# Kernel optimization log

Hardware: AMD Instinct MI355X
Metric: run time of the kernel (lower is better)

## Reference

```python
import jax, jax.numpy as jnp
import numpy as np

B, SI, ST, D = 2, 1024, 512, 2048
H, KV, HD = 16, 4, 128
E, F, TOPK = 8, 1024, 2
EPS = 1e-6


def _rms(x, w):
    x32 = x.astype(jnp.float32)
    y = x32 * jax.lax.rsqrt(jnp.mean(x32 * x32, axis=-1, keepdims=True) + EPS)
    return y.astype(x.dtype) * w


def _rope(x, cos, sin):
    # x: [B,S,h,HD]; cos/sin: [S,HD//2]. Complex-pair rotation (use_real=False path):
    # pairs (x[2i], x[2i+1]) treated as complex, multiplied by e^{i theta}.
    xr, xi = x[..., 0::2], x[..., 1::2]
    c = cos[None, :, None, :]
    s = sin[None, :, None, :]
    out_r = xr * c - xi * s
    out_i = xr * s + xi * c
    return jnp.stack([out_r, out_i], axis=-1).reshape(x.shape)


def setup_inputs() -> dict:
    key = jax.random.key(0)
    ks = jax.random.split(key, 12)
    def w(k, shape, fan_in):
        return jax.random.normal(k, shape, jnp.float32) * (fan_in ** -0.5)
    pos_i = np.arange(SI)[:, None].astype(np.float32)
    pos_t = np.arange(ST)[:, None].astype(np.float32)
    inv = (1.0 / (10000.0 ** (np.arange(0, HD, 2).astype(np.float32) / HD)))[None, :]
    return {
        'hidden_states': jax.random.normal(ks[0], (B, SI, D), jnp.float32),
        'encoder_hidden_states': jax.random.normal(ks[1], (B, ST, D), jnp.float32),
        'img_cos': jnp.asarray(np.cos(pos_i * inv), jnp.float32),
        'img_sin': jnp.asarray(np.sin(pos_i * inv), jnp.float32),
        'txt_cos': jnp.asarray(np.cos(pos_t * inv), jnp.float32),
        'txt_sin': jnp.asarray(np.sin(pos_t * inv), jnp.float32),
        'norm1_w': jnp.ones((D,), jnp.float32),
        'norm2_w': jnp.ones((D,), jnp.float32),
        'wq': w(ks[2], (D, H * HD), D),
        'wk': w(ks[3], (D, KV * HD), D),
        'wv': w(ks[4], (D, KV * HD), D),
        'wk_txt': w(ks[5], (D, KV * HD), D),
        'wv_txt': w(ks[6], (D, KV * HD), D),
        'wo': w(ks[7], (H * HD, D), H * HD),
        'q_norm_w': jnp.ones((HD,), jnp.float32),
        'k_norm_w': jnp.ones((HD,), jnp.float32),
        'added_k_norm_w': jnp.ones((HD,), jnp.float32),
        'router_w': w(ks[8], (D, E), D),
        'gate_up_proj': w(ks[9], (E, D, 2 * F), D),
        'down_proj': w(ks[10], (E, F, D), F),
    }


def reference(hidden_states, encoder_hidden_states, img_cos, img_sin, txt_cos, txt_sin,
              norm1_w, norm2_w, wq, wk, wv, wk_txt, wv_txt, wo,
              q_norm_w, k_norm_w, added_k_norm_w, router_w, gate_up_proj, down_proj):
    h = hidden_states
    # ---- cross-attn: image queries over concat(image, text) K/V, GQA + RoPE ----
    x = _rms(h, norm1_w)
    q = _rms((x @ wq).reshape(B, SI, H, HD), q_norm_w)
    k_img = _rms((x @ wk).reshape(B, SI, KV, HD), k_norm_w)
    v_img = (x @ wv).reshape(B, SI, KV, HD)
    q = _rope(q, img_cos, img_sin)
    k_img = _rope(k_img, img_cos, img_sin)
    k_txt = _rms((encoder_hidden_states @ wk_txt).reshape(B, ST, KV, HD), added_k_norm_w)
    k_txt = _rope(k_txt, txt_cos, txt_sin)
    v_txt = (encoder_hidden_states @ wv_txt).reshape(B, ST, KV, HD)
    k = jnp.concatenate([k_img, k_txt], axis=1)  # [B, SI+ST, KV, HD]
    v = jnp.concatenate([v_img, v_txt], axis=1)
    k = jnp.repeat(k, H // KV, axis=2)  # GQA repeat_interleave over heads
    v = jnp.repeat(v, H // KV, axis=2)
    scores = jnp.einsum('bqhd,bkhd->bhqk', q, k) * (HD ** -0.5)
    attn = jax.nn.softmax(scores.astype(jnp.float32), axis=-1).astype(q.dtype)
    o = jnp.einsum('bhqk,bkhd->bqhd', attn, v).reshape(B, SI, H * HD)
    h = h + o @ wo
    # ---- MoE: top-k router + packed SwiGLU experts ----
    xt = _rms(h, norm2_w).reshape(B * SI, D)
    probs = jax.nn.softmax((xt @ router_w).astype(jnp.float32), axis=-1)
    topv, topi = jax.lax.top_k(probs, TOPK)
    topv = topv / jnp.sum(topv, axis=-1, keepdims=True)
    wgt = jnp.sum(jax.nn.one_hot(topi, E, dtype=xt.dtype) * topv.astype(xt.dtype)[..., None], axis=1)  # [T,E]
    gate_up = jnp.einsum('td,edg->teg', xt, gate_up_proj)  # [T,E,2F]
    gate, up = gate_up[..., :F], gate_up[..., F:]
    act = jax.nn.silu(gate) * up
    eo = jnp.einsum('tef,efd->ted', act, down_proj)  # [T,E,D]
    moe_out = jnp.einsum('te,ted->td', wgt, eo).reshape(B, SI, D)
    return h + moe_out
```

## Files before the change

kernel.cpp:

```cpp
#include <hip/hip_runtime.h>


typedef __attribute__((ext_vector_type(8))) __bf16 bf16x8;
typedef __attribute__((ext_vector_type(8))) unsigned short u16x8;
typedef __attribute__((ext_vector_type(4))) float f32x4;

__device__ __forceinline__ unsigned short f2bf(float x) {
  unsigned u = __builtin_bit_cast(unsigned, x);
  u += 0x7fffu + ((u >> 16) & 1u);
  return (unsigned short)(u >> 16);
}
__device__ __forceinline__ float bf2f(unsigned short b) {
  return __builtin_bit_cast(float, ((unsigned)b) << 16);
}

__device__ __forceinline__ void glds16(const unsigned short* g, unsigned short* l) {
  __builtin_amdgcn_global_load_lds(
      (const __attribute__((address_space(1))) void*)g,
      (__attribute__((address_space(3))) void*)l, 16, 0, 0);
}

__device__ __forceinline__ int xcd_swz(int orig, int nwg) {
  int q = nwg >> 3, r = nwg & 7;
  int xcd = orig & 7, idx = orig >> 3;
  int base = (xcd < r) ? xcd * (q + 1) : r * (q + 1) + (xcd - r) * q;
  return base + idx;
}

struct CvtJobs {
  const float* src[8];
  unsigned short* dst[8];
  int K[8];
  int N[8];
  int off[9];
};

__global__ __launch_bounds__(256) void convert_all(CvtJobs jb)
{
  __shared__ unsigned short T[64][66];
  const int bid = blockIdx.x;
  int j = 0;
  #pragma unroll
  for (int i = 0; i < 8; ++i) if (bid >= jb.off[i + 1]) j = i + 1;
  const int local = bid - jb.off[j];
  const int K = jb.K[j], N = jb.N[j];
  const int kb = K >> 6, nb = N >> 6;
  const int kt = local % kb;
  const int rest = local / kb;
  const int nt = rest % nb, zi = rest / nb;
  const float* Wz = jb.src[j] + (size_t)zi * K * N;
  unsigned short* WTz = jb.dst[j] + (size_t)zi * K * N;
  const int k0 = kt * 64, n0 = nt * 64;
  const int tid = threadIdx.x;
  #pragma unroll
  for (int i = tid; i < 64 * 16; i += 256) {
    int k = i >> 4, n4 = (i & 15) * 4;
    float4 v = *(const float4*)&Wz[(size_t)(k0 + k) * N + n0 + n4];
    T[n4 + 0][k] = f2bf(v.x);
    T[n4 + 1][k] = f2bf(v.y);
    T[n4 + 2][k] = f2bf(v.z);
    T[n4 + 3][k] = f2bf(v.w);
  }
  __syncthreads();
  #pragma unroll
  for (int i = tid; i < 64 * 8; i += 256) {
    int n = i >> 3, k8 = (i & 7) * 8;
    *(u16x8*)&WTz[(size_t)(n0 + n) * K + k0 + k8] = *(const u16x8*)&T[n][k8];
  }
}

__global__ __launch_bounds__(256) void gemm_bb(
    const unsigned short* __restrict__ A, const unsigned short* __restrict__ BT,
    float* __restrict__ C, const float* __restrict__ resid,
    int M, int N, int K)
{
  __shared__ unsigned short As[2][128 * 64];
  __shared__ unsigned short Bs[2][128 * 64];
  const int mb = M >> 7;
  const int w = xcd_swz(blockIdx.x, gridDim.x);
  const int bm = (w % mb) * 128, bn = (w / mb) * 128;
  const int tid = threadIdx.x, lane = tid & 63, wid = tid >> 6;
  const int wm = (wid >> 1) * 64, wn = (wid & 1) * 64;
  const int l16 = lane & 15, g4 = lane >> 4;
  const int rseg = lane >> 3;
  const int csw  = ((lane & 7) ^ rseg) * 8;
  const unsigned short* aSrc[4];
  const unsigned short* bSrc[4];
  #pragma unroll
  for (int p = 0; p < 4; ++p) {
    int row = (p * 4 + wid) * 8 + rseg;
    aSrc[p] = A  + (size_t)(bm + row) * K + csw;
    bSrc[p] = BT + (size_t)(bn + row) * K + csw;
  }
  f32x4 acc[4][4] = {};
  const int NT = K >> 6;
  #pragma unroll
  for (int p = 0; p < 4; ++p) glds16(aSrc[p], &As[0][(p * 4 + wid) * 512]);
  #pragma unroll
  for (int p = 0; p < 4; ++p) glds16(bSrc[p], &Bs[0][(p * 4 + wid) * 512]);
  for (int t = 0; t < NT; ++t) {
    const int cur = t & 1;
    if (t + 1 < NT) {
      const int k0 = (t + 1) << 6;
      #pragma unroll
      for (int p = 0; p < 4; ++p) glds16(aSrc[p] + k0, &As[cur ^ 1][(p * 4 + wid) * 512]);
      #pragma unroll
      for (int p = 0; p < 4; ++p) glds16(bSrc[p] + k0, &Bs[cur ^ 1][(p * 4 + wid) * 512]);
      asm volatile("s_waitcnt vmcnt(8)" ::: "memory");
    } else {
      asm volatile("s_waitcnt vmcnt(0)" ::: "memory");
    }
    __builtin_amdgcn_s_barrier();
    __builtin_amdgcn_sched_barrier(0);
    const unsigned short* ab = &As[cur][0];
    const unsigned short* bb = &Bs[cur][0];
    #pragma unroll
    for (int ks = 0; ks < 2; ++ks) {
      bf16x8 af[4], bf[4];
      #pragma unroll
      for (int i = 0; i < 4; ++i) {
        int ra = wm + i * 16 + l16;
        int rb = wn + i * 16 + l16;
        int ch = ((ks * 4 + g4) ^ (l16 & 7)) * 8;
        af[i] = *(const bf16x8*)&ab[ra * 64 + ch];
        bf[i] = *(const bf16x8*)&bb[rb * 64 + ch];
      }
      #pragma unroll
      for (int mi = 0; mi < 4; ++mi)
        #pragma unroll
        for (int ni = 0; ni < 4; ++ni)
          acc[mi][ni] = __builtin_amdgcn_mfma_f32_16x16x32_bf16(af[mi], bf[ni], acc[mi][ni], 0, 0, 0);
    }
    __builtin_amdgcn_sched_barrier(0);
    __builtin_amdgcn_s_barrier();
  }
  const int r4 = g4 * 4;
  #pragma unroll
  for (int mi = 0; mi < 4; ++mi)
    #pragma unroll
    for (int ni = 0; ni < 4; ++ni)
      #pragma unroll
      for (int r = 0; r < 4; ++r) {
        int row = bm + wm + mi * 16 + r4 + r;
        int col = bn + wn + ni * 16 + l16;
        float v = acc[mi][ni][r];
        if (resid) v += resid[(size_t)row * N + col];
        C[(size_t)row * N + col] = v;
      }
}

__global__ __launch_bounds__(512, 1) void gemm_moe_256sk(
    const unsigned short* __restrict__ A, const unsigned short* __restrict__ BTall,
    float* __restrict__ C0, float* __restrict__ C1,
    const int* __restrict__ counts, const int* __restrict__ offsets,
    const int* __restrict__ pair_token, const unsigned short* __restrict__ zbuf,
    int gather, int K, int N)
{
  const int w = xcd_swz(blockIdx.x, gridDim.x);
  const int e = w >> 7;
  const int local = w & 127;
  const int bm = ((local >> 4) & 7) * 256;
  const int kh = (local >> 3) & 1;
  const int bn = (local & 7) * 256;
  const int cnt = counts[e];
  if (bm >= cnt) return;
  const int base = offsets[e];
  const int Kh = K >> 1;
  float* __restrict__ C = kh ? C1 : C0;
  __shared__ unsigned short As[256 * 64];
  __shared__ unsigned short Bs[256 * 64];
  __shared__ int rowmap[256];
  const int tid = threadIdx.x, lane = tid & 63, wid = tid >> 6;
  const int wr = wid >> 2, wc = wid & 3;
  const int l16 = lane & 15, g4 = lane >> 4;
  const int rseg = lane >> 3;
  const int csw  = ((lane & 7) ^ rseg) * 8;
  if (tid < 256) {
    int lr = bm + tid;
    rowmap[tid] = (lr < cnt) ? (gather ? pair_token[base + lr] : base + lr) : -1;
  }
  __syncthreads();
  const unsigned short* BT = BTall + (size_t)e * N * K;
  const unsigned short* aSrc[4];
  const unsigned short* bSrc[4];
  int aOk[4];
  #pragma unroll
  for (int p = 0; p < 4; ++p) {
    int row = (p * 8 + wid) * 8 + rseg;
    int tok = rowmap[row];
    aOk[p] = (tok >= 0);
    aSrc[p] = aOk[p] ? (A + (size_t)tok * K + kh * Kh + csw) : (zbuf + csw);
    bSrc[p] = BT + (size_t)(bn + row) * K + kh * Kh + csw;
  }
  f32x4 acc[8][4] = {};
  const int NT = Kh >> 6;
  for (int t = 0; t < NT; ++t) {
    const int k0 = t << 6;
    #pragma unroll
    for (int p = 0; p < 4; ++p)
      glds16(aSrc[p] + (aOk[p] ? k0 : 0), &As[(p * 8 + wid) * 512]);
    #pragma unroll
    for (int p = 0; p < 4; ++p)
      glds16(bSrc[p] + k0, &Bs[(p * 8 + wid) * 512]);
    __syncthreads();
    #pragma unroll
    for (int ks = 0; ks < 2; ++ks) {
      const int ch = ((ks * 4 + g4) ^ (l16 & 7)) * 8;
      bf16x8 bf[4];
      #pragma unroll
      for (int j = 0; j < 4; ++j)
        bf[j] = *(const bf16x8*)&Bs[(wc * 64 + j * 16 + l16) * 64 + ch];
      #pragma unroll
      for (int mi = 0; mi < 8; ++mi) {
        bf16x8 af = *(const bf16x8*)&As[(wr * 128 + mi * 16 + l16) * 64 + ch];
        #pragma unroll
        for (int ni = 0; ni < 4; ++ni)
          acc[mi][ni] = __builtin_amdgcn_mfma_f32_16x16x32_bf16(af, bf[ni], acc[mi][ni], 0, 0, 0);
      }
    }
    __syncthreads();
  }
  const int r4 = g4 * 4;
  #pragma unroll
  for (int mi = 0; mi < 8; ++mi)
    #pragma unroll
    for (int ni = 0; ni < 4; ++ni)
      #pragma unroll
      for (int r = 0; r < 4; ++r) {
        int lrow = bm + wr * 128 + mi * 16 + r4 + r;
        int col  = bn + wc * 64 + ni * 16 + l16;
        if (lrow < cnt)
          C[(size_t)(base + lrow) * N + col] = acc[mi][ni][r];
      }
}

__global__ __launch_bounds__(256) void rmsnorm_rows(
    const float* __restrict__ in, const float* __restrict__ w,
    unsigned short* __restrict__ out)
{
  const int row = blockIdx.x;
  const int tid = threadIdx.x;
  const float* x = in + (size_t)row * 2048;
  float4 a = *(const float4*)&x[tid * 8];
  float4 b = *(const float4*)&x[tid * 8 + 4];
  float s = a.x*a.x + a.y*a.y + a.z*a.z + a.w*a.w
          + b.x*b.x + b.y*b.y + b.z*b.z + b.w*b.w;
  #pragma unroll
  for (int off = 1; off < 64; off <<= 1) s += __shfl_xor(s, off);
  __shared__ float red[4];
  if ((tid & 63) == 0) red[tid >> 6] = s;
  __syncthreads();
  float inv = rsqrtf((red[0] + red[1] + red[2] + red[3]) * (1.f / 2048.f) + 1e-6f);
  float4 wa = *(const float4*)&w[tid * 8];
  float4 wb = *(const float4*)&w[tid * 8 + 4];
  unsigned short* o = out + (size_t)row * 2048 + tid * 8;
  o[0] = f2bf(a.x * inv * wa.x); o[1] = f2bf(a.y * inv * wa.y);
  o[2] = f2bf(a.z * inv * wa.z); o[3] = f2bf(a.w * inv * wa.w);
  o[4] = f2bf(b.x * inv * wb.x); o[5] = f2bf(b.y * inv * wb.y);
  o[6] = f2bf(b.z * inv * wb.z); o[7] = f2bf(b.w * inv * wb.w);
}

__global__ __launch_bounds__(256) void rmsnorm_router(
    const float* __restrict__ in, const float* __restrict__ w,
    unsigned short* __restrict__ xt, const float* __restrict__ rw,
    int* __restrict__ topi, float* __restrict__ topw, int* __restrict__ counts)
{
  const int row = blockIdx.x;
  const int tid = threadIdx.x, lane = tid & 63, wid = tid >> 6;
  const float* x = in + (size_t)row * 2048;
  float4 a = *(const float4*)&x[tid * 8];
  float4 b = *(const float4*)&x[tid * 8 + 4];
  float s = a.x*a.x + a.y*a.y + a.z*a.z + a.w*a.w
          + b.x*b.x + b.y*b.y + b.z*b.z + b.w*b.w;
  #pragma unroll
  for (int off = 1; off < 64; off <<= 1) s += __shfl_xor(s, off);
  __shared__ float red[4];
  __shared__ float rl[4][8];
  if (lane == 0) red[wid] = s;
  __syncthreads();
  float inv = rsqrtf((red[0] + red[1] + red[2] + red[3]) * (1.f / 2048.f) + 1e-6f);
  float4 wa = *(const float4*)&w[tid * 8];
  float4 wb = *(const float4*)&w[tid * 8 + 4];
  float y[8] = {a.x * inv * wa.x, a.y * inv * wa.y, a.z * inv * wa.z, a.w * inv * wa.w,
                b.x * inv * wb.x, b.y * inv * wb.y, b.z * inv * wb.z, b.w * inv * wb.w};
  unsigned short* o = xt + (size_t)row * 2048 + tid * 8;
  #pragma unroll
  for (int j = 0; j < 8; ++j) o[j] = f2bf(y[j]);
  float lg[8] = {};
  #pragma unroll
  for (int j = 0; j < 8; ++j) {
    int d = tid * 8 + j;
    const float4 r0 = *(const float4*)&rw[d * 8];
    const float4 r1 = *(const float4*)&rw[d * 8 + 4];
    lg[0] += y[j] * r0.x; lg[1] += y[j] * r0.y; lg[2] += y[j] * r0.z; lg[3] += y[j] * r0.w;
    lg[4] += y[j] * r1.x; lg[5] += y[j] * r1.y; lg[6] += y[j] * r1.z; lg[7] += y[j] * r1.w;
  }
  #pragma unroll
  for (int e = 0; e < 8; ++e)
    #pragma unroll
    for (int off = 1; off < 64; off <<= 1) lg[e] += __shfl_xor(lg[e], off);
  if (lane == 0) {
    #pragma unroll
    for (int e = 0; e < 8; ++e) rl[wid][e] = lg[e];
  }
  __syncthreads();
  if (tid == 0) {
    float l[8];
    #pragma unroll
    for (int e = 0; e < 8; ++e) l[e] = rl[0][e] + rl[1][e] + rl[2][e] + rl[3][e];
    float v0 = l[0]; int e0 = 0;
    #pragma unroll
    for (int e = 1; e < 8; ++e) if (l[e] > v0) { v0 = l[e]; e0 = e; }
    float v1 = -1e30f; int e1 = 0;
    #pragma unroll
    for (int e = 0; e < 8; ++e) if (e != e0 && l[e] > v1) { v1 = l[e]; e1 = e; }
    float x1 = expf(v1 - v0);
    float w0 = 1.f / (1.f + x1);
    float w1 = x1 / (1.f + x1);
    topi[2 * row] = e0; topi[2 * row + 1] = e1;
    topw[2 * row] = w0; topw[2 * row + 1] = w1;
    atomicAdd(&counts[e0], 1);
    atomicAdd(&counts[e1], 1);
  }
}

__global__ __launch_bounds__(256) void f32_to_bf16_k(
    const float* __restrict__ in, unsigned short* __restrict__ out, int n)
{
  int i = (blockIdx.x * 256 + threadIdx.x) * 4;
  if (i + 3 < n) {
    float4 v = *(const float4*)&in[i];
    out[i + 0] = f2bf(v.x); out[i + 1] = f2bf(v.y);
    out[i + 2] = f2bf(v.z); out[i + 3] = f2bf(v.w);
  }
}

__global__ __launch_bounds__(256) void prep_all(
    const float* __restrict__ qkvC, const float* __restrict__ kvtC,
    const float* __restrict__ q_norm_w, const float* __restrict__ k_norm_w,
    const float* __restrict__ added_k_norm_w,
    const float* __restrict__ img_cos, const float* __restrict__ img_sin,
    const float* __restrict__ txt_cos, const float* __restrict__ txt_sin,
    unsigned short* __restrict__ qb, unsigned short* __restrict__ kbuf,
    unsigned short* __restrict__ vbuf, float scale)
{
  const int bid = blockIdx.x;
  const int tid = threadIdx.x, lane = tid & 63;
  int job, rel;
  if (bid < 8192)       { job = 0; rel = bid; }
  else if (bid < 10240) { job = 1; rel = bid - 8192; }
  else if (bid < 11264) { job = 2; rel = bid - 10240; }
  else if (bid < 13312) { job = 3; rel = bid - 11264; }
  else                  { job = 4; rel = bid - 13312; }
  const float* src_base; int ld, S, NH, soff, st;
  const float* nw = nullptr; const float* cosT = nullptr; const float* sinT = nullptr;
  unsigned short* dst; float premul = 1.f; bool dorope;
  switch (job) {
    case 0: src_base = qkvC;        ld = 3072; S = 1024; NH = 16; soff = 0;    st = 1024;
            nw = q_norm_w;       cosT = img_cos; sinT = img_sin; dst = qb;   premul = scale; dorope = true;  break;
    case 1: src_base = qkvC + 2048; ld = 3072; S = 1024; NH = 4;  soff = 0;    st = 1536;
            nw = k_norm_w;       cosT = img_cos; sinT = img_sin; dst = kbuf;                 dorope = true;  break;
    case 2: src_base = kvtC;        ld = 1024; S = 512;  NH = 4;  soff = 1024; st = 1536;
            nw = added_k_norm_w; cosT = txt_cos; sinT = txt_sin; dst = kbuf;                 dorope = true;  break;
    case 3: src_base = qkvC + 2560; ld = 3072; S = 1024; NH = 4;  soff = 0;    st = 1536;
            dst = vbuf; dorope = false; break;
    default:src_base = kvtC + 512;  ld = 1024; S = 512;  NH = 4;  soff = 1024; st = 1536;
            dst = vbuf; dorope = false; break;
  }
  int rowid = rel * 4 + (tid >> 6);
  int b = rowid / (S * NH);
  int rem = rowid % (S * NH);
  int s = rem / NH, h = rem % NH;
  const float* src = src_base + (size_t)(b * S + s) * ld + h * 128;
  float2 xv = *(const float2*)&src[lane * 2];
  float orr, oi;
  if (dorope) {
    float ss = xv.x * xv.x + xv.y * xv.y;
    #pragma unroll
    for (int off = 1; off < 64; off <<= 1) ss += __shfl_xor(ss, off);
    float inv = rsqrtf(ss * (1.f / 128.f) + 1e-6f);
    float yr = xv.x * inv * nw[lane * 2];
    float yi = xv.y * inv * nw[lane * 2 + 1];
    float c  = cosT[s * 64 + lane], sn = sinT[s * 64 + lane];
    orr = (yr * c - yi * sn) * premul;
    oi  = (yr * sn + yi * c) * premul;
  } else {
    orr = xv.x; oi = xv.y;
  }
  unsigned short* d = dst + ((size_t)(b * NH + h) * st + (s + soff)) * 128;
  d[lane * 2]     = f2bf(orr);
  d[lane * 2 + 1] = f2bf(oi);
}

__global__ __launch_bounds__(512) void attn_kernel(
    const unsigned short* __restrict__ q,
    const unsigned short* __restrict__ kbuf,
    const unsigned short* __restrict__ vbuf,
    unsigned short* __restrict__ o)
{
  const int SK = 1536;
  const int w = xcd_swz(blockIdx.x, gridDim.x);
  const int bh = w >> 3;
  const int b = bh >> 4, h = bh & 15, kvh = h >> 2;
  const int q0 = (w & 7) * 128;
  const int tid = threadIdx.x, lane = tid & 63, wid = tid >> 6;
  const int l16 = lane & 15, kb = (lane >> 4) * 8, r4 = (lane >> 4) * 4;
  __shared__ unsigned short KsL[64 * 128];
  __shared__ unsigned short VTL[128 * 64];
  __shared__ unsigned short PsL[8 * 16 * 64];
  const int sr0 = tid >> 4;
  const int scc = (tid & 15) * 8;

  const unsigned short* qrow =
      q + ((size_t)(b * 16 + h) * 1024 + q0 + wid * 16 + l16) * 128;
  bf16x8 qf[4];
  #pragma unroll
  for (int ks = 0; ks < 4; ++ks) qf[ks] = *(const bf16x8*)&qrow[ks * 32 + kb];
  float mrow[4] = {-1e30f, -1e30f, -1e30f, -1e30f};
  float lrow[4] = {0.f, 0.f, 0.f, 0.f};
  f32x4 oacc[8] = {};
  const unsigned short* kb_base = kbuf + (size_t)(b * 4 + kvh) * SK * 128;
  const unsigned short* vb_base = vbuf + (size_t)(b * 4 + kvh) * SK * 128;

  u16x8 k0[2], v0[2], k1[2], v1[2];

#define ATT_LOAD(kr, vr, kt1)                                                 \
  {                                                                           \
    _Pragma("unroll")                                                         \
    for (int i = 0; i < 2; ++i) {                                             \
      kr[i] = *(const u16x8*)&kb_base[(size_t)((kt1) + sr0 + 32 * i) * 128 + scc]; \
      vr[i] = *(const u16x8*)&vb_base[(size_t)((kt1) + sr0 + 32 * i) * 128 + scc]; \
    }                                                                         \
  }

#define ATT_STAGE(kr, vr)                                                     \
  {                                                                           \
    _Pragma("unroll")                                                         \
    for (int i = 0; i < 2; ++i) {                                             \
      int rr = sr0 + 32 * i;                                                  \
      *(u16x8*)&KsL[rr * 128 + (((scc >> 3) ^ (rr & 7)) << 3)] = kr[i];       \
      _Pragma("unroll")                                                       \
      for (int j = 0; j < 8; ++j)                                             \
        VTL[(scc + j) * 64 + ((((rr >> 3) ^ ((scc + j) >> 3)) & 7) << 3) + (rr & 7)] = vr[i][j]; \
    }                                                                         \
  }

  auto compute = [&]() {
    f32x4 sacc[4] = {};
    __builtin_amdgcn_s_setprio(1);
    #pragma unroll
    for (int ks = 0; ks < 4; ++ks) {
      #pragma unroll
      for (int ni = 0; ni < 4; ++ni) {
        int rr = ni * 16 + l16;
        bf16x8 kf = *(const bf16x8*)
            &KsL[rr * 128 + ((((ks * 32 + kb) >> 3) ^ (rr & 7)) << 3)];
        sacc[ni] = __builtin_amdgcn_mfma_f32_16x16x32_bf16(qf[ks], kf, sacc[ni], 0, 0, 0);
      }
    }
    __builtin_amdgcn_s_setprio(0);
    float pv[4][4], alpha[4];
    #pragma unroll
    for (int r = 0; r < 4; ++r) {
      float tm = fmaxf(fmaxf(sacc[0][r], sacc[1][r]), fmaxf(sacc[2][r], sacc[3][r]));
      #pragma unroll
      for (int off = 1; off < 16; off <<= 1) tm = fmaxf(tm, __shfl_xor(tm, off));
      float mn = fmaxf(mrow[r], tm);
      alpha[r] = __expf(mrow[r] - mn);
      float s = 0.f;
      #pragma unroll
      for (int ni = 0; ni < 4; ++ni) {
        float p = __expf(sacc[ni][r] - mn);
        pv[ni][r] = p; s += p;
      }
      #pragma unroll
      for (int off = 1; off < 16; off <<= 1) s += __shfl_xor(s, off);
      lrow[r] = lrow[r] * alpha[r] + s;
      mrow[r] = mn;
    }
    #pragma unroll
    for (int ni = 0; ni < 8; ++ni)
      #pragma unroll
      for (int r = 0; r < 4; ++r) oacc[ni][r] *= alpha[r];
    #pragma unroll
    for (int ni = 0; ni < 4; ++ni)
      #pragma unroll
      for (int r = 0; r < 4; ++r) {
        int row = r4 + r, col = ni * 16 + l16;
        PsL[wid * 1024 + row * 64 + ((((col >> 3) ^ (row & 7)) & 7) << 3) + (col & 7)]
            = f2bf(pv[ni][r]);
      }
    asm volatile("s_waitcnt lgkmcnt(0)" ::: "memory");
    __builtin_amdgcn_sched_barrier(0);
    __builtin_amdgcn_s_setprio(1);
    #pragma unroll
    for (int ks = 0; ks < 2; ++ks) {
      bf16x8 pf = *(const bf16x8*)
          &PsL[wid * 1024 + l16 * 64 + ((((ks * 32 + kb) >> 3) ^ (l16 & 7)) << 3)];
      #pragma unroll
      for (int ni = 0; ni < 8; ++ni) {
        int d = ni * 16 + l16;
        bf16x8 vf = *(const bf16x8*)
            &VTL[d * 64 + ((((ks * 32 + kb) >> 3) ^ ((d >> 3) & 7)) << 3)];
        oacc[ni] = __builtin_amdgcn_mfma_f32_16x16x32_bf16(pf, vf, oacc[ni], 0, 0, 0);
      }
    }
    __builtin_amdgcn_s_setprio(0);
  };

  ATT_LOAD(k0, v0, 0);
  for (int t = 0; t < 24; t += 2) {
    ATT_STAGE(k0, v0);
    ATT_LOAD(k1, v1, (t + 1) * 64);
    asm volatile("s_waitcnt lgkmcnt(0)" ::: "memory");
    __builtin_amdgcn_s_barrier();
    __builtin_amdgcn_sched_barrier(0);
    compute();
    __builtin_amdgcn_sched_barrier(0);
    __builtin_amdgcn_s_barrier();
    ATT_STAGE(k1, v1);
    if (t + 2 < 24) ATT_LOAD(k0, v0, (t + 2) * 64);
    asm volatile("s_waitcnt lgkmcnt(0)" ::: "memory");
    __builtin_amdgcn_s_barrier();
    __builtin_amdgcn_sched_barrier(0);
    compute();
    __builtin_amdgcn_sched_barrier(0);
    __builtin_amdgcn_s_barrier();
  }
#undef ATT_LOAD
#undef ATT_STAGE

  #pragma unroll
  for (int ni = 0; ni < 8; ++ni)
    #pragma unroll
    for (int r = 0; r < 4; ++r) {
      float val = oacc[ni][r] / lrow[r];
      size_t row = (size_t)b * 1024 + q0 + wid * 16 + r4 + r;
      o[row * 2048 + h * 128 + ni * 16 + l16] = f2bf(val);
    }
}

__global__ void scan_offsets(const int* __restrict__ counts, int* __restrict__ offsets)
{
  if (threadIdx.x == 0 && blockIdx.x == 0) {
    int a = 0;
    for (int e = 0; e < 8; ++e) { offsets[e] = a; a += counts[e]; }
    offsets[8] = a;
  }
}

__global__ __launch_bounds__(256) void scatter_pairs(
    const int* __restrict__ topi, const int* __restrict__ offsets,
    int* __restrict__ fill, int* __restrict__ pair_token, int* __restrict__ token_slot)
{
  int t = blockIdx.x * 256 + threadIdx.x;
  if (t >= 2048) return;
  #pragma unroll
  for (int k = 0; k < 2; ++k) {
    int e = topi[2 * t + k];
    int slot = offsets[e] + atomicAdd(&fill[e], 1);
    pair_token[slot] = t;
    token_slot[2 * t + k] = slot;
  }
}

__global__ __launch_bounds__(256) void act_silu2(
    const float* __restrict__ gu0, const float* __restrict__ gu1,
    unsigned short* __restrict__ act)
{
  int p = blockIdx.x;
  int c = threadIdx.x * 4;
  float4 g0 = *(const float4*)&gu0[(size_t)p * 2048 + c];
  float4 g1 = *(const float4*)&gu1[(size_t)p * 2048 + c];
  float4 u0 = *(const float4*)&gu0[(size_t)p * 2048 + 1024 + c];
  float4 u1 = *(const float4*)&gu1[(size_t)p * 2048 + 1024 + c];
  float gg[4] = {g0.x + g1.x, g0.y + g1.y, g0.z + g1.z, g0.w + g1.w};
  float uu[4] = {u0.x + u1.x, u0.y + u1.y, u0.z + u1.z, u0.w + u1.w};
  #pragma unroll
  for (int j = 0; j < 4; ++j) {
    float a = gg[j] / (1.f + __expf(-gg[j])) * uu[j];
    act[(size_t)p * 1024 + c + j] = f2bf(a);
  }
}

__global__ __launch_bounds__(256) void moe_combine2(
    float* __restrict__ out, const float* __restrict__ eo0,
    const float* __restrict__ eo1,
    const int* __restrict__ token_slot, const float* __restrict__ topw)
{
  int t = blockIdx.x;
  int c = threadIdx.x * 8;
  int s0 = token_slot[2 * t], s1 = token_slot[2 * t + 1];
  float w0 = topw[2 * t], w1 = topw[2 * t + 1];
  #pragma unroll
  for (int j0 = 0; j0 < 8; j0 += 4) {
    float4 a0 = *(const float4*)&eo0[(size_t)s0 * 2048 + c + j0];
    float4 a1 = *(const float4*)&eo1[(size_t)s0 * 2048 + c + j0];
    float4 b0 = *(const float4*)&eo0[(size_t)s1 * 2048 + c + j0];
    float4 b1 = *(const float4*)&eo1[(size_t)s1 * 2048 + c + j0];
    float4 v = *(const float4*)&out[(size_t)t * 2048 + c + j0];
    v.x += w0 * (a0.x + a1.x) + w1 * (b0.x + b1.x);
    v.y += w0 * (a0.y + a1.y) + w1 * (b0.y + b1.y);
    v.z += w0 * (a0.z + a1.z) + w1 * (b0.z + b1.z);
    v.w += w0 * (a0.w + a1.w) + w1 * (b0.w + b1.w);
    *(float4*)&out[(size_t)t * 2048 + c + j0] = v;
  }
}

extern "C" void kernel_launch(void* const* d_in, const int* in_sizes, int n_in,
                              void* d_out, int out_size, void* d_ws, size_t ws_size,
                              hipStream_t stream)
{
  const float* hidden  = (const float*)d_in[0];
  const float* enc     = (const float*)d_in[1];
  const float* img_cos = (const float*)d_in[2];
  const float* img_sin = (const float*)d_in[3];
  const float* txt_cos = (const float*)d_in[4];
  const float* txt_sin = (const float*)d_in[5];
  const float* norm1_w = (const float*)d_in[6];
  const float* norm2_w = (const float*)d_in[7];
  const float* wq      = (const float*)d_in[8];
  const float* wk      = (const float*)d_in[9];
  const float* wv      = (const float*)d_in[10];
  const float* wk_txt  = (const float*)d_in[11];
  const float* wv_txt  = (const float*)d_in[12];
  const float* wo      = (const float*)d_in[13];
  const float* q_norm_w       = (const float*)d_in[14];
  const float* k_norm_w       = (const float*)d_in[15];
  const float* added_k_norm_w = (const float*)d_in[16];
  const float* router_w       = (const float*)d_in[17];
  const float* gate_up_proj   = (const float*)d_in[18];
  const float* down_proj      = (const float*)d_in[19];
  float* out = (float*)d_out;

  char* ws = (char*)d_ws;
  size_t off = 0;
  auto alloc = [&](size_t bytes) {
    void* p = ws + off;
    off += (bytes + 255) & ~(size_t)255;
    return p;
  };
  unsigned short* wqkvT  = (unsigned short*)alloc(3072ULL * 2048 * 2);
  unsigned short* wkvtT  = (unsigned short*)alloc(1024ULL * 2048 * 2);
  unsigned short* woT    = (unsigned short*)alloc(2048ULL * 2048 * 2);
  unsigned short* gupT   = (unsigned short*)alloc(8ULL * 2048 * 2048 * 2);
  unsigned short* dnT    = (unsigned short*)alloc(8ULL * 2048 * 1024 * 2);
  unsigned short* x_bf   = (unsigned short*)alloc(2048ULL * 2048 * 2);
  unsigned short* enc_bf = (unsigned short*)alloc(1024ULL * 2048 * 2);
  float* qkvC = (float*)alloc(4096ULL * 2048 * 4);
  float* gu0  = qkvC;
  float* gu1  = (float*)alloc(4096ULL * 2048 * 4);
  float* kvtC = (float*)alloc(1024ULL * 1024 * 4);
  unsigned short* qb   = (unsigned short*)alloc(2048ULL * 2048 * 2);
  unsigned short* kbuf = (unsigned short*)alloc(2ULL * 4 * 1536 * 128 * 2);
  unsigned short* vbuf = (unsigned short*)alloc(2ULL * 4 * 1536 * 128 * 2);
  unsigned short* obuf = (unsigned short*)alloc(2048ULL * 2048 * 2);
  unsigned short* act  = obuf;
  unsigned short* xt   = (unsigned short*)alloc(2048ULL * 2048 * 2);
  int*   ctrl  = (int*)alloc(64 * sizeof(int));
  int*   topi  = (int*)alloc(4096 * 4);
  float* topw  = (float*)alloc(4096 * 4);
  int*   tslot = (int*)alloc(4096 * 4);
  int*   ptok  = (int*)alloc(4096 * 4);
  unsigned short* zbuf = (unsigned short*)alloc(256);
  int* counts = ctrl, * fill = ctrl + 8, * offsets = ctrl + 16;

  hipMemsetAsync(ctrl, 0, 64, stream);
  hipMemsetAsync(zbuf, 0, 256, stream);

  const float scale = 0.08838834764831845f;

  CvtJobs jb;
  jb.src[0] = wq;     jb.dst[0] = wqkvT;                  jb.K[0] = 2048; jb.N[0] = 2048;
  jb.src[1] = wk;     jb.dst[1] = wqkvT + 2048ULL * 2048; jb.K[1] = 2048; jb.N[1] = 512;
  jb.src[2] = wv;     jb.dst[2] = wqkvT + 2560ULL * 2048; jb.K[2] = 2048; jb.N[2] = 512;
  jb.src[3] = wk_txt; jb.dst[3] = wkvtT;                  jb.K[3] = 2048; jb.N[3] = 512;
  jb.src[4] = wv_txt; jb.dst[4] = wkvtT + 512ULL * 2048;  jb.K[4] = 2048; jb.N[4] = 512;
  jb.src[5] = wo;     jb.dst[5] = woT;                    jb.K[5] = 2048; jb.N[5] = 2048;
  jb.src[6] = gate_up_proj; jb.dst[6] = gupT;             jb.K[6] = 2048; jb.N[6] = 2048;
  jb.src[7] = down_proj;    jb.dst[7] = dnT;              jb.K[7] = 1024; jb.N[7] = 2048;
  jb.off[0] = 0;     jb.off[1] = 1024;  jb.off[2] = 1280; jb.off[3] = 1536;
  jb.off[4] = 1792;  jb.off[5] = 2048;  jb.off[6] = 3072; jb.off[7] = 11264;
  jb.off[8] = 15360;
  convert_all<<<15360, 256, 0, stream>>>(jb);

  rmsnorm_rows<<<2048, 256, 0, stream>>>(hidden, norm1_w, x_bf);
  f32_to_bf16_k<<<2048, 256, 0, stream>>>(enc, enc_bf, 1024 * 2048);

  gemm_bb<<<384, 256, 0, stream>>>(x_bf, wqkvT, qkvC, nullptr, 2048, 3072, 2048);
  gemm_bb<<<64, 256, 0, stream>>>(enc_bf, wkvtT, kvtC, nullptr, 1024, 1024, 2048);

  prep_all<<<14336, 256, 0, stream>>>(qkvC, kvtC, q_norm_w, k_norm_w, added_k_norm_w,
                                      img_cos, img_sin, txt_cos, txt_sin,
                                      qb, kbuf, vbuf, scale);

  attn_kernel<<<256, 512, 0, stream>>>(qb, kbuf, vbuf, obuf);

  gemm_bb<<<256, 256, 0, stream>>>(obuf, woT, out, hidden, 2048, 2048, 2048);

  rmsnorm_router<<<2048, 256, 0, stream>>>(out, norm2_w, xt, router_w,
                                           topi, topw, counts);
  scan_offsets<<<1, 64, 0, stream>>>(counts, offsets);
  scatter_pairs<<<8, 256, 0, stream>>>(topi, offsets, fill, ptok, tslot);

  gemm_moe_256sk<<<1024, 512, 0, stream>>>(xt, gupT, gu0, gu1,
                                           counts, offsets, ptok, zbuf, 1, 2048, 2048);
  act_silu2<<<4096, 256, 0, stream>>>(gu0, gu1, act);
  gemm_moe_256sk<<<1024, 512, 0, stream>>>(act, dnT, gu0, gu1,
                                           counts, offsets, ptok, zbuf, 0, 1024, 2048);
  moe_combine2<<<2048, 256, 0, stream>>>(out, gu0, gu1, tslot, topw);
}
```

Before: 562.9 us.

## Fuse QK RMSNorm, RoPE and KV scatter into QKV GEMM epilogue

Removes the separate prep_all kernel and the fp32 qkvC/kvtC intermediates. The QKV and text KV GEMMs now apply per-head RMSNorm, rotary embedding, scaling and the bf16 scatter into q/k/v layouts directly in their epilogue. Because each 128-wide N tile is exactly one head, row sums of squares can be reduced through shared memory. This cuts a large fp32 write and read round trip plus a launch, at the cost of a heavier GEMM epilogue with scattered 2-byte stores.

```diff
diff --git a/kernel.cpp b/kernel.cpp
--- a/kernel.cpp
+++ b/kernel.cpp
@@ -69,10 +69,24 @@
   }
 }
 
+struct Epi {
+  unsigned short* qb;
+  unsigned short* kbuf;
+  unsigned short* vbuf;
+  const float* q_nw;
+  const float* k_nw;
+  const float* kt_nw;
+  const float* icos;
+  const float* isin;
+  const float* tcos;
+  const float* tsin;
+  float scale;
+};
+
 __global__ __launch_bounds__(256) void gemm_bb(
     const unsigned short* __restrict__ A, const unsigned short* __restrict__ BT,
     float* __restrict__ C, const float* __restrict__ resid,
-    int M, int N, int K)
+    int M, int N, int K, int mode, Epi ep)
 {
   __shared__ unsigned short As[2][128 * 64];
   __shared__ unsigned short Bs[2][128 * 64];
@@ -135,18 +149,103 @@
     __builtin_amdgcn_s_barrier();
   }
   const int r4 = g4 * 4;
+
+  if (mode == 0) {
+    #pragma unroll
+    for (int mi = 0; mi < 4; ++mi)
+      #pragma unroll
+      for (int ni = 0; ni < 4; ++ni)
+        #pragma unroll
+        for (int r = 0; r < 4; ++r) {
+          int row = bm + wm + mi * 16 + r4 + r;
+          int col = bn + wn + ni * 16 + l16;
+          float v = acc[mi][ni][r];
+          if (resid) v += resid[(size_t)row * N + col];
+          C[(size_t)row * N + col] = v;
+        }
+    return;
+  }
+
+  const int bt = bn >> 7;
+  unsigned short* dst;
+  const float* nw = nullptr;
+  const float* cosT = nullptr;
+  const float* sinT = nullptr;
+  int h, NH, st, soff, vkind = 0, shift;
+  float premul = 1.f;
+  int S;
+  if (mode == 1) {
+    S = 1024; shift = 10;
+    if (bt < 16)      { h = bt;      dst = ep.qb;   nw = ep.q_nw; cosT = ep.icos; sinT = ep.isin;
+                        NH = 16; st = 1024; soff = 0; premul = ep.scale; }
+    else if (bt < 20) { h = bt - 16; dst = ep.kbuf; nw = ep.k_nw; cosT = ep.icos; sinT = ep.isin;
+                        NH = 4;  st = 1536; soff = 0; }
+    else              { h = bt - 20; dst = ep.vbuf; vkind = 1; NH = 4; st = 1536; soff = 0; }
+  } else {
+    S = 512; shift = 9;
+    if (bt < 4) { h = bt;     dst = ep.kbuf; nw = ep.kt_nw; cosT = ep.tcos; sinT = ep.tsin;
+                  NH = 4; st = 1536; soff = 1024; }
+    else        { h = bt - 4; dst = ep.vbuf; vkind = 1; NH = 4; st = 1536; soff = 1024; }
+  }
+
+  if (vkind) {
+    #pragma unroll
+    for (int mi = 0; mi < 4; ++mi)
+      #pragma unroll
+      for (int ni = 0; ni < 4; ++ni)
+        #pragma unroll
+        for (int r = 0; r < 4; ++r) {
+          int row = wm + mi * 16 + r4 + r;
+          int d   = wn + ni * 16 + l16;
+          int token = bm + row;
+          int srow = token & (S - 1), bidx = token >> shift;
+          dst[((size_t)(bidx * NH + h) * st + srow + soff) * 128 + d] = f2bf(acc[mi][ni][r]);
+        }
+    return;
+  }
+
+  float* ssb = (float*)&As[0][0];
+  float ssp[4][4];
   #pragma unroll
   for (int mi = 0; mi < 4; ++mi)
     #pragma unroll
-    for (int ni = 0; ni < 4; ++ni)
-      #pragma unroll
-      for (int r = 0; r < 4; ++r) {
-        int row = bm + wm + mi * 16 + r4 + r;
-        int col = bn + wn + ni * 16 + l16;
-        float v = acc[mi][ni][r];
-        if (resid) v += resid[(size_t)row * N + col];
-        C[(size_t)row * N + col] = v;
+    for (int r = 0; r < 4; ++r) {
+      float v = 0.f;
+      #pragma unroll
+      for (int ni = 0; ni < 4; ++ni) v += acc[mi][ni][r] * acc[mi][ni][r];
+      #pragma unroll
+      for (int off = 1; off < 16; off <<= 1) v += __shfl_xor(v, off);
+      ssp[mi][r] = v;
+    }
+  __syncthreads();
+  if (l16 == 0) {
+    #pragma unroll
+    for (int mi = 0; mi < 4; ++mi)
+      #pragma unroll
+      for (int r = 0; r < 4; ++r)
+        ssb[(wid & 1) * 128 + wm + mi * 16 + r4 + r] = ssp[mi][r];
+  }
+  __syncthreads();
+  #pragma unroll
+  for (int mi = 0; mi < 4; ++mi)
+    #pragma unroll
+    for (int r = 0; r < 4; ++r) {
+      int row = wm + mi * 16 + r4 + r;
+      float tot = ssb[row] + ssb[128 + row];
+      float inv = rsqrtf(tot * (1.f / 128.f) + 1e-6f);
+      int token = bm + row;
+      int srow = token & (S - 1), bidx = token >> shift;
+      #pragma unroll
+      for (int ni = 0; ni < 4; ++ni) {
+        int d = wn + ni * 16 + l16;
+        float y = acc[mi][ni][r] * inv * nw[d];
+        float part = __shfl_xor(y, 1);
+        float c  = cosT[srow * 64 + (d >> 1)];
+        float sn = sinT[srow * 64 + (d >> 1)];
+        float outv = (d & 1) ? (part * sn + y * c) : (y * c - part * sn);
+        dst[((size_t)(bidx * NH + h) * st + srow + soff) * 128 + d] = f2bf(outv * premul);
       }
+    }
 }
 
 __global__ __launch_bounds__(512, 1) void gemm_moe_256sk(
@@ -335,63 +434,6 @@
   }
 }
 
-__global__ __launch_bounds__(256) void prep_all(
-    const float* __restrict__ qkvC, const float* __restrict__ kvtC,
-    const float* __restrict__ q_norm_w, const float* __restrict__ k_norm_w,
-    const float* __restrict__ added_k_norm_w,
-    const float* __restrict__ img_cos, const float* __restrict__ img_sin,
-    const float* __restrict__ txt_cos, const float* __restrict__ txt_sin,
-    unsigned short* __restrict__ qb, unsigned short* __restrict__ kbuf,
-    unsigned short* __restrict__ vbuf, float scale)
-{
-  const int bid = blockIdx.x;
-  const int tid = threadIdx.x, lane = tid & 63;
-  int job, rel;
-  if (bid < 8192)       { job = 0; rel = bid; }
-  else if (bid < 10240) { job = 1; rel = bid - 8192; }
-  else if (bid < 11264) { job = 2; rel = bid - 10240; }
-  else if (bid < 13312) { job = 3; rel = bid - 11264; }
-  else                  { job = 4; rel = bid - 13312; }
-  const float* src_base; int ld, S, NH, soff, st;
-  const float* nw = nullptr; const float* cosT = nullptr; const float* sinT = nullptr;
-  unsigned short* dst; float premul = 1.f; bool dorope;
-  switch (job) {
-    case 0: src_base = qkvC;        ld = 3072; S = 1024; NH = 16; soff = 0;    st = 1024;
-            nw = q_norm_w;       cosT = img_cos; sinT = img_sin; dst = qb;   premul = scale; dorope = true;  break;
-    case 1: src_base = qkvC + 2048; ld = 3072; S = 1024; NH = 4;  soff = 0;    st = 1536;
-            nw = k_norm_w;       cosT = img_cos; sinT = img_sin; dst = kbuf;                 dorope = true;  break;
-    case 2: src_base = kvtC;        ld = 1024; S = 512;  NH = 4;  soff = 1024; st = 1536;
-            nw = added_k_norm_w; cosT = txt_cos; sinT = txt_sin; dst = kbuf;                 dorope = true;  break;
-    case 3: src_base = qkvC + 2560; ld = 3072; S = 1024; NH = 4;  soff = 0;    st = 1536;
-            dst = vbuf; dorope = false; break;
-    default:src_base = kvtC + 512;  ld = 1024; S = 512;  NH = 4;  soff = 1024; st = 1536;
-            dst = vbuf; dorope = false; break;
-  }
-  int rowid = rel * 4 + (tid >> 6);
-  int b = rowid / (S * NH);
-  int rem = rowid % (S * NH);
-  int s = rem / NH, h = rem % NH;
-  const float* src = src_base + (size_t)(b * S + s) * ld + h * 128;
-  float2 xv = *(const float2*)&src[lane * 2];
-  float orr, oi;
-  if (dorope) {
-    float ss = xv.x * xv.x + xv.y * xv.y;
-    #pragma unroll
-    for (int off = 1; off < 64; off <<= 1) ss += __shfl_xor(ss, off);
-    float inv = rsqrtf(ss * (1.f / 128.f) + 1e-6f);
-    float yr = xv.x * inv * nw[lane * 2];
-    float yi = xv.y * inv * nw[lane * 2 + 1];
-    float c  = cosT[s * 64 + lane], sn = sinT[s * 64 + lane];
-    orr = (yr * c - yi * sn) * premul;
-    oi  = (yr * sn + yi * c) * premul;
-  } else {
-    orr = xv.x; oi = xv.y;
-  }
-  unsigned short* d = dst + ((size_t)(b * NH + h) * st + (s + soff)) * 128;
-  d[lane * 2]     = f2bf(orr);
-  d[lane * 2 + 1] = f2bf(oi);
-}
-
 __global__ __launch_bounds__(512) void attn_kernel(
     const unsigned short* __restrict__ q,
     const unsigned short* __restrict__ kbuf,
@@ -647,10 +689,8 @@
   unsigned short* dnT    = (unsigned short*)alloc(8ULL * 2048 * 1024 * 2);
   unsigned short* x_bf   = (unsigned short*)alloc(2048ULL * 2048 * 2);
   unsigned short* enc_bf = (unsigned short*)alloc(1024ULL * 2048 * 2);
-  float* qkvC = (float*)alloc(4096ULL * 2048 * 4);
-  float* gu0  = qkvC;
+  float* gu0  = (float*)alloc(4096ULL * 2048 * 4);
   float* gu1  = (float*)alloc(4096ULL * 2048 * 4);
-  float* kvtC = (float*)alloc(1024ULL * 1024 * 4);
   unsigned short* qb   = (unsigned short*)alloc(2048ULL * 2048 * 2);
   unsigned short* kbuf = (unsigned short*)alloc(2ULL * 4 * 1536 * 128 * 2);
   unsigned short* vbuf = (unsigned short*)alloc(2ULL * 4 * 1536 * 128 * 2);
@@ -687,16 +727,18 @@
   rmsnorm_rows<<<2048, 256, 0, stream>>>(hidden, norm1_w, x_bf);
   f32_to_bf16_k<<<2048, 256, 0, stream>>>(enc, enc_bf, 1024 * 2048);
 
-  gemm_bb<<<384, 256, 0, stream>>>(x_bf, wqkvT, qkvC, nullptr, 2048, 3072, 2048);
-  gemm_bb<<<64, 256, 0, stream>>>(enc_bf, wkvtT, kvtC, nullptr, 1024, 1024, 2048);
-
-  prep_all<<<14336, 256, 0, stream>>>(qkvC, kvtC, q_norm_w, k_norm_w, added_k_norm_w,
-                                      img_cos, img_sin, txt_cos, txt_sin,
-                                      qb, kbuf, vbuf, scale);
+  Epi ep;
+  ep.qb = qb; ep.kbuf = kbuf; ep.vbuf = vbuf;
+  ep.q_nw = q_norm_w; ep.k_nw = k_norm_w; ep.kt_nw = added_k_norm_w;
+  ep.icos = img_cos; ep.isin = img_sin; ep.tcos = txt_cos; ep.tsin = txt_sin;
+  ep.scale = scale;
+
+  gemm_bb<<<384, 256, 0, stream>>>(x_bf, wqkvT, nullptr, nullptr, 2048, 3072, 2048, 1, ep);
+  gemm_bb<<<64, 256, 0, stream>>>(enc_bf, wkvtT, nullptr, nullptr, 1024, 1024, 2048, 2, ep);
 
   attn_kernel<<<256, 512, 0, stream>>>(qb, kbuf, vbuf, obuf);
 
-  gemm_bb<<<256, 256, 0, stream>>>(obuf, woT, out, hidden, 2048, 2048, 2048);
+  gemm_bb<<<256, 256, 0, stream>>>(obuf, woT, out, hidden, 2048, 2048, 2048, 0, ep);
 
   rmsnorm_router<<<2048, 256, 0, stream>>>(out, norm2_w, xt, router_w,
                                            topi, topw, counts);
```

Result: no change. 558.7 us (-0.7%).
